# Kernel tuning notes

Measured on AMD Instinct MI355X. Metric: run time of the kernel, lower is better.

## Reference

```python
import jax, jax.numpy as jnp
import numpy as np

BSZ, T, D_IN, P, H, D_OUT = 8, 4096, 512, 256, 256, 512


def setup_inputs() -> dict:
    key = jax.random.key(0)
    ks = jax.random.split(key, 8)
    x_seq = jax.random.normal(ks[0], (BSZ, T, D_IN), dtype=jnp.float32)
    # stable diagonal transition: |a| < 1 so the 4096-step recurrence does not blow up
    a = jax.random.uniform(ks[1], (H,), minval=-0.99, maxval=0.99, dtype=jnp.float32)
    B = jax.random.normal(ks[2], (P, H), dtype=jnp.float32) * 0.05
    C = jax.random.normal(ks[3], (H, P), dtype=jnp.float32) * 0.05
    Wi = jax.random.normal(ks[4], (P, D_IN), dtype=jnp.float32) * 0.05
    bi = jax.random.normal(ks[5], (P,), dtype=jnp.float32) * 0.05
    Wo = jax.random.normal(ks[6], (D_OUT, P), dtype=jnp.float32) * 0.05
    bo = jax.random.normal(ks[7], (D_OUT,), dtype=jnp.float32) * 0.05
    return {"x_seq": x_seq, "a": a, "B": B, "C": C, "Wi": Wi, "bi": bi, "Wo": Wo, "bo": bo}


def reference(x_seq, a, B, C, Wi, bi, Wo, bo):
    # proj_in + relu (eqx.nn.Linear: y = W @ x + b), vmapped over batch and time
    x_proj = jax.nn.relu(jnp.einsum("btd,pd->btp", x_seq, Wi) + bi)  # [Bsz,T,P]
    # precompute driving input u_t = B^T x_t for every step
    u = jnp.einsum("btp,ph->bth", x_proj, B)  # [Bsz,T,H]
    u_t = jnp.swapaxes(u, 0, 1)  # [T,Bsz,H] (scan over time)

    def step(h, u_step):  # h: [Bsz,H]
        h = a * h + u_step
        return h, h

    h0 = jnp.zeros((x_seq.shape[0], a.shape[0]), dtype=x_seq.dtype)
    _, hs = jax.lax.scan(step, h0, u_t)  # hs: [T,Bsz,H]
    # y_t = C^T h_t, then proj_out
    y_seq = jnp.einsum("tbh,hp->btp", hs, C)  # [Bsz,T,P]
    y_out = jnp.einsum("btp,op->bto", y_seq, Wo) + bo  # [Bsz,T,D_out]
    return y_out
```

## Files before the change

### kernel.cpp

```cpp
#include <hip/hip_runtime.h>

#define BSZN 8
#define TT 4096
#define DIN 512
#define PP 256
#define HHH 256
#define DOUT 512
#define LCH 64
#define NCH (TT / LCH)
#define NBLK (BSZN * NCH)
#define XPS 264
#define AST 136

typedef __attribute__((ext_vector_type(8))) short bf16x8;
typedef __attribute__((ext_vector_type(4))) float f32x4;

#define GLOBAL_AS __attribute__((address_space(1)))
#define LDS_AS __attribute__((address_space(3)))

static __device__ __forceinline__ void gld_lds16(const void* g, void* l) {
  __builtin_amdgcn_global_load_lds((const GLOBAL_AS unsigned int*)g,
                                   (LDS_AS unsigned int*)l, 16, 0, 0);
}

static __device__ __forceinline__ unsigned short f2bf(float x) {
  union { float f; unsigned u; } t{x};
  unsigned r = t.u + 0x7fffu + ((t.u >> 16) & 1u);
  return (unsigned short)(r >> 16);
}


__global__ __launch_bounds__(256) void prep_k(
    const float* __restrict__ Wi, const float* __restrict__ Wo,
    const float* __restrict__ Cm, const float* __restrict__ Bm,
    unsigned short* __restrict__ Wi_t, unsigned short* __restrict__ B_t,
    unsigned short* __restrict__ C_t, unsigned short* __restrict__ Wo_t) {
  const int b = blockIdx.x, tid = threadIdx.x;
  if (b < 128) {
    const int idx = b * 1024 + tid * 4;
    const int row = idx >> 9, d = idx & 511;
    const float4 v = *(const float4*)(Wi + idx);
    uint2 w;
    w.x = (unsigned)f2bf(v.x) | ((unsigned)f2bf(v.y) << 16);
    w.y = (unsigned)f2bf(v.z) | ((unsigned)f2bf(v.w) << 16);
    const int tile = d >> 5, kc = (d >> 3) & 3, s = (kc + (row >> 1)) & 3;
    *(uint2*)(Wi_t + tile * 8192 + row * 32 + s * 8 + (d & 7)) = w;
  } else if (b < 192) {
    const int f = (b - 128) * 256 + tid;
    const int p = f >> 6, h = (f & 63) * 4;
    const float4 v = *(const float4*)(Bm + (size_t)p * HHH + h);
    const float vv[4] = {v.x, v.y, v.z, v.w};
    const int tile = p >> 5, kc = (p >> 3) & 3;
#pragma unroll
    for (int j = 0; j < 4; ++j) {
      const int row = h + j, s = (kc + (row >> 1)) & 3;
      B_t[tile * 8192 + row * 32 + s * 8 + (p & 7)] = f2bf(vv[j]);
    }
  } else if (b < 256) {
    const int f = (b - 192) * 256 + tid;
    const int h = f >> 6, p = (f & 63) * 4;
    const float4 v = *(const float4*)(Cm + (size_t)h * PP + p);
    const float vv[4] = {v.x, v.y, v.z, v.w};
    const int tile = h >> 5, kc = (h >> 3) & 3;
#pragma unroll
    for (int j = 0; j < 4; ++j) {
      const int row = p + j, s = (kc + (row >> 1)) & 3;
      C_t[tile * 8192 + row * 32 + s * 8 + (h & 7)] = f2bf(vv[j]);
    }
  } else {
    const int idx = (b - 256) * 1024 + tid * 4;
    const int o = idx >> 8, p = idx & 255;
    const float4 v = *(const float4*)(Wo + idx);
    uint2 w;
    w.x = (unsigned)f2bf(v.x) | ((unsigned)f2bf(v.y) << 16);
    w.y = (unsigned)f2bf(v.z) | ((unsigned)f2bf(v.w) << 16);
    const int tile = p >> 5, kc = (p >> 3) & 3, s = (kc + (o >> 1)) & 3;
    *(uint2*)(Wo_t + tile * 16384 + o * 32 + s * 8 + (p & 7)) = w;
  }
}

__global__ __launch_bounds__(256, 2) void s4_scan(
    const float* __restrict__ x, const float* __restrict__ a,
    const unsigned short* __restrict__ Wi_t, const float* __restrict__ bi,
    const unsigned short* __restrict__ B_t, float* __restrict__ hs0_g,
    float* __restrict__ carry_g) {
  __shared__ alignas(16) char smem[66560];
  char* As = smem;
  unsigned short* xp = (unsigned short*)smem;
  char* TB = smem + 33792;

  const int tid = threadIdx.x, wave = tid >> 6, lane = tid & 63;
  const int l15 = lane & 15, q = lane >> 4;
  const int bc = blockIdx.x;
  const size_t row0 = (size_t)bc * LCH;
  const int wc = wave * 64;

  int wrot[4];
#pragma unroll
  for (int ni = 0; ni < 4; ++ni) {
    const int r = wc + ni * 16 + l15;
    wrot[ni] = r * 64 + (((q + (r >> 1)) & 3) << 4);
  }
  int afb[4];
#pragma unroll
  for (int mi = 0; mi < 4; ++mi) afb[mi] = (mi * 16 + l15) * AST + q * 16;
  int xpb[4];
#pragma unroll
  for (int mi = 0; mi < 4; ++mi) xpb[mi] = (mi * 16 + l15) * XPS + q * 8;

  const int sbase = wave * 4096 + lane * 16;

  f32x4 acc[4][4];
#pragma unroll
  for (int i = 0; i < 4; ++i)
#pragma unroll
    for (int j = 0; j < 4; ++j) acc[i][j] = f32x4{0.f, 0.f, 0.f, 0.f};

  float4 xv[4];
#pragma unroll
  for (int i = 0; i < 4; ++i) {
    const int f = i * 256 + tid;
    xv[i] = *(const float4*)(x + (row0 + (f >> 4)) * DIN + (f & 15) * 4);
  }
  for (int t = 0; t < 8; ++t) {
#pragma unroll
    for (int i = 0; i < 4; ++i) {
      const int f = i * 256 + tid;
      uint2 w;
      w.x = (unsigned)f2bf(xv[i].x) | ((unsigned)f2bf(xv[i].y) << 16);
      w.y = (unsigned)f2bf(xv[i].z) | ((unsigned)f2bf(xv[i].w) << 16);
      *(uint2*)(As + (f >> 4) * AST + (f & 15) * 8) = w;
    }
    {
      const char* gw = (const char*)Wi_t + t * 32768 + sbase;
#pragma unroll
      for (int i = 0; i < 4; ++i) {
        gld_lds16(gw + i * 1024, TB + sbase + i * 1024);
        gld_lds16(gw + 16384 + i * 1024, TB + 16384 + sbase + i * 1024);
      }
    }
    __syncthreads();
    if (t < 7) {
#pragma unroll
      for (int i = 0; i < 4; ++i) {
        const int f = i * 256 + tid;
        xv[i] = *(const float4*)(x + (row0 + (f >> 4)) * DIN + (t + 1) * 64 +
                                 (f & 15) * 4);
      }
    }
    bf16x8 af[4][2], bfv[4][2];
#pragma unroll
    for (int mi = 0; mi < 4; ++mi) {
      af[mi][0] = *(const bf16x8*)(As + afb[mi]);
      af[mi][1] = *(const bf16x8*)(As + afb[mi] + 64);
    }
#pragma unroll
    for (int ni = 0; ni < 4; ++ni) {
      bfv[ni][0] = *(const bf16x8*)(TB + wrot[ni]);
      bfv[ni][1] = *(const bf16x8*)(TB + 16384 + wrot[ni]);
    }
#pragma unroll
    for (int kk = 0; kk < 2; ++kk)
#pragma unroll
      for (int mi = 0; mi < 4; ++mi)
#pragma unroll
        for (int ni = 0; ni < 4; ++ni)
          acc[mi][ni] = __builtin_amdgcn_mfma_f32_16x16x32_bf16(
              af[mi][kk], bfv[ni][kk], acc[mi][ni], 0, 0, 0);
    __syncthreads();
  }

  {
    const char* gw = (const char*)B_t + sbase;
#pragma unroll
    for (int i = 0; i < 4; ++i) {
      gld_lds16(gw + i * 1024, TB + sbase + i * 1024);
      gld_lds16(gw + 16384 + i * 1024, TB + 16384 + sbase + i * 1024);
    }
  }

#pragma unroll
  for (int ni = 0; ni < 4; ++ni) {
    const int col = wc + ni * 16 + l15;
    const float bb = bi[col];
#pragma unroll
    for (int mi = 0; mi < 4; ++mi)
#pragma unroll
      for (int reg = 0; reg < 4; ++reg) {
        const int row = mi * 16 + q * 4 + reg;
        xp[row * XPS + col] = f2bf(fmaxf(acc[mi][ni][reg] + bb, 0.f));
      }
  }

#pragma unroll
  for (int i = 0; i < 4; ++i)
#pragma unroll
    for (int j = 0; j < 4; ++j) acc[i][j] = f32x4{0.f, 0.f, 0.f, 0.f};
  for (int t = 0; t < 4; ++t) {
    if (t > 0) {
      const char* gw = (const char*)B_t + t * 32768 + sbase;
#pragma unroll
      for (int i = 0; i < 4; ++i) {
        gld_lds16(gw + i * 1024, TB + sbase + i * 1024);
        gld_lds16(gw + 16384 + i * 1024, TB + 16384 + sbase + i * 1024);
      }
    }
    __syncthreads();
    bf16x8 af[4][2], bfv[4][2];
#pragma unroll
    for (int mi = 0; mi < 4; ++mi) {
      af[mi][0] = *(const bf16x8*)(xp + xpb[mi] + t * 64);
      af[mi][1] = *(const bf16x8*)(xp + xpb[mi] + t * 64 + 32);
    }
#pragma unroll
    for (int ni = 0; ni < 4; ++ni) {
      bfv[ni][0] = *(const bf16x8*)(TB + wrot[ni]);
      bfv[ni][1] = *(const bf16x8*)(TB + 16384 + wrot[ni]);
    }
#pragma unroll
    for (int kk = 0; kk < 2; ++kk)
#pragma unroll
      for (int mi = 0; mi < 4; ++mi)
#pragma unroll
        for (int ni = 0; ni < 4; ++ni)
          acc[mi][ni] = __builtin_amdgcn_mfma_f32_16x16x32_bf16(
              af[mi][kk], bfv[ni][kk], acc[mi][ni], 0, 0, 0);
    __syncthreads();
  }

  float aC[4], Wz[4];
#pragma unroll
  for (int ni = 0; ni < 4; ++ni) aC[ni] = a[wc + ni * 16 + l15];
#pragma unroll
  for (int ni = 0; ni < 4; ++ni) {
    const float A = aC[ni];
    const float A2 = A * A, A4 = A2 * A2, A8 = A4 * A4, A16 = A8 * A8;
    const float A4q = ((q & 1) ? A4 : 1.f) * ((q & 2) ? A8 : 1.f);
    float W = 0.f;
#pragma unroll
    for (int mi = 0; mi < 4; ++mi) {
      f32x4 v = acc[mi][ni];
      v.y = fmaf(A, v.x, v.y);
      v.z = fmaf(A, v.y, v.z);
      v.w = fmaf(A, v.z, v.w);
      const float E = v.w;
      const float E0 = __shfl(E, l15, 64);
      const float E1 = __shfl(E, l15 + 16, 64);
      const float E2 = __shfl(E, l15 + 32, 64);
      const float E3 = __shfl(E, l15 + 48, 64);
      const float s1 = E0, s2 = fmaf(A4, s1, E1), s3 = fmaf(A4, s2, E2);
      const float s4 = fmaf(A4, s3, E3);
      const float Sq = (q == 0) ? 0.f : (q == 1) ? s1 : (q == 2) ? s2 : s3;
      const float sin_ = fmaf(A4q, W, Sq);
      v.x = fmaf(A, sin_, v.x);
      v.y = fmaf(A2, sin_, v.y);
      v.z = fmaf(A2 * A, sin_, v.z);
      v.w = fmaf(A4, sin_, v.w);
      acc[mi][ni] = v;
      W = fmaf(A16, W, s4);
    }
    Wz[ni] = W;
  }
  if (q == 0) {
#pragma unroll
    for (int ni = 0; ni < 4; ++ni)
      carry_g[(size_t)bc * HHH + wc + ni * 16 + l15] = Wz[ni];
  }
#pragma unroll
  for (int ni = 0; ni < 4; ++ni) {
    const int col = wc + ni * 16 + l15;
#pragma unroll
    for (int mi = 0; mi < 4; ++mi)
#pragma unroll
      for (int reg = 0; reg < 4; ++reg) {
        const int row = mi * 16 + q * 4 + reg;
        hs0_g[(row0 + row) * HHH + col] = acc[mi][ni][reg];
      }
  }
}

__global__ __launch_bounds__(256) void s4_prefix(
    const float* __restrict__ a, const float* __restrict__ carry_g,
    float* __restrict__ P_g) {
  const int b = blockIdx.x, t = threadIdx.x;
  float A = a[t];
#pragma unroll
  for (int j = 0; j < 6; ++j) A *= A;
  const float* cg = carry_g + (size_t)b * NCH * HHH + t;
  float* pg = P_g + (size_t)b * NCH * HHH + t;
  float cv[NCH];
#pragma unroll
  for (int c = 0; c < NCH; ++c) cv[c] = cg[(size_t)c * HHH];
  float P = 0.f;
#pragma unroll
  for (int c = 0; c < NCH; ++c) {
    pg[(size_t)c * HHH] = P;
    P = fmaf(A, P, cv[c]);
  }
}

__global__ __launch_bounds__(256, 2) void s4_out(
    const float* __restrict__ a, const float* __restrict__ hs0_g,
    const float* __restrict__ P_g, const unsigned short* __restrict__ C_t,
    const unsigned short* __restrict__ Wo_t, const float* __restrict__ bo,
    float* __restrict__ out) {
  __shared__ alignas(16) char smem[66560];
  unsigned short* hsL = (unsigned short*)smem;
  char* TB = smem + 33792;

  const int tid = threadIdx.x, wave = tid >> 6, lane = tid & 63;
  const int l15 = lane & 15, q = lane >> 4;
  const int bc = blockIdx.x;
  const size_t row0 = (size_t)bc * LCH;
  const int wc = wave * 64;

  int wrot[4];
#pragma unroll
  for (int ni = 0; ni < 4; ++ni) {
    const int r = wc + ni * 16 + l15;
    wrot[ni] = r * 64 + (((q + (r >> 1)) & 3) << 4);
  }
  int crot[2][4];
#pragma unroll
  for (int g = 0; g < 2; ++g)
#pragma unroll
    for (int ni = 0; ni < 4; ++ni) {
      const int r = wave * 128 + g * 64 + ni * 16 + l15;
      crot[g][ni] = r * 64 + (((q + (r >> 1)) & 3) << 4);
    }
  int xpb[4];
#pragma unroll
  for (int mi = 0; mi < 4; ++mi) xpb[mi] = (mi * 16 + l15) * XPS + q * 8;

  const int sbase = wave * 4096 + lane * 16;

  {
    const char* gw = (const char*)C_t + sbase;
#pragma unroll
    for (int i = 0; i < 4; ++i) {
      gld_lds16(gw + i * 1024, TB + sbase + i * 1024);
      gld_lds16(gw + 16384 + i * 1024, TB + 16384 + sbase + i * 1024);
    }
  }

  f32x4 acc[4][4];
#pragma unroll
  for (int ni = 0; ni < 4; ++ni) {
    const int col = wc + ni * 16 + l15;
#pragma unroll
    for (int mi = 0; mi < 4; ++mi)
#pragma unroll
      for (int reg = 0; reg < 4; ++reg)
        acc[mi][ni][reg] = hs0_g[(row0 + mi * 16 + q * 4 + reg) * HHH + col];
  }
#pragma unroll
  for (int ni = 0; ni < 4; ++ni) {
    const int col = wc + ni * 16 + l15;
    const float A = a[col];
    const float P = P_g[(size_t)bc * HHH + col];
    const float A2 = A * A, A4 = A2 * A2, A8 = A4 * A4, A16 = A8 * A8;
    const float A4q = ((q & 1) ? A4 : 1.f) * ((q & 2) ? A8 : 1.f);
    float fm = A4q * A * P;
#pragma unroll
    for (int mi = 0; mi < 4; ++mi) {
      f32x4 v = acc[mi][ni];
      v.x += fm;
      v.y = fmaf(A, fm, v.y);
      v.z = fmaf(A2, fm, v.z);
      v.w = fmaf(A2 * A, fm, v.w);
      acc[mi][ni] = v;
      fm *= A16;
    }
  }
#pragma unroll
  for (int ni = 0; ni < 4; ++ni) {
    const int col = wc + ni * 16 + l15;
#pragma unroll
    for (int mi = 0; mi < 4; ++mi)
#pragma unroll
      for (int reg = 0; reg < 4; ++reg)
        hsL[(mi * 16 + q * 4 + reg) * XPS + col] = f2bf(acc[mi][ni][reg]);
  }

#pragma unroll
  for (int i = 0; i < 4; ++i)
#pragma unroll
    for (int j = 0; j < 4; ++j) acc[i][j] = f32x4{0.f, 0.f, 0.f, 0.f};
  for (int t = 0; t < 4; ++t) {
    if (t > 0) {
      const char* gw = (const char*)C_t + t * 32768 + sbase;
#pragma unroll
      for (int i = 0; i < 4; ++i) {
        gld_lds16(gw + i * 1024, TB + sbase + i * 1024);
        gld_lds16(gw + 16384 + i * 1024, TB + 16384 + sbase + i * 1024);
      }
    }
    __syncthreads();
    bf16x8 af[4][2], bfv[4][2];
#pragma unroll
    for (int mi = 0; mi < 4; ++mi) {
      af[mi][0] = *(const bf16x8*)(hsL + xpb[mi] + t * 64);
      af[mi][1] = *(const bf16x8*)(hsL + xpb[mi] + t * 64 + 32);
    }
#pragma unroll
    for (int ni = 0; ni < 4; ++ni) {
      bfv[ni][0] = *(const bf16x8*)(TB + wrot[ni]);
      bfv[ni][1] = *(const bf16x8*)(TB + 16384 + wrot[ni]);
    }
#pragma unroll
    for (int kk = 0; kk < 2; ++kk)
#pragma unroll
      for (int mi = 0; mi < 4; ++mi)
#pragma unroll
        for (int ni = 0; ni < 4; ++ni)
          acc[mi][ni] = __builtin_amdgcn_mfma_f32_16x16x32_bf16(
              af[mi][kk], bfv[ni][kk], acc[mi][ni], 0, 0, 0);
    __syncthreads();
  }

  {
    const char* gw = (const char*)Wo_t + wave * 8192 + lane * 16;
#pragma unroll
    for (int i = 0; i < 8; ++i)
      gld_lds16(gw + i * 1024, TB + wave * 8192 + lane * 16 + i * 1024);
  }
#pragma unroll
  for (int ni = 0; ni < 4; ++ni) {
    const int col = wc + ni * 16 + l15;
#pragma unroll
    for (int mi = 0; mi < 4; ++mi)
#pragma unroll
      for (int reg = 0; reg < 4; ++reg)
        hsL[(mi * 16 + q * 4 + reg) * XPS + col] = f2bf(acc[mi][ni][reg]);
  }

  f32x4 oacc[2][4][4];
#pragma unroll
  for (int g = 0; g < 2; ++g)
#pragma unroll
    for (int i = 0; i < 4; ++i)
#pragma unroll
      for (int j = 0; j < 4; ++j) oacc[g][i][j] = f32x4{0.f, 0.f, 0.f, 0.f};
  for (int t = 0; t < 8; ++t) {
    if (t > 0) {
      const char* gw = (const char*)Wo_t + t * 32768 + wave * 8192 + lane * 16;
#pragma unroll
      for (int i = 0; i < 8; ++i)
        gld_lds16(gw + i * 1024, TB + wave * 8192 + lane * 16 + i * 1024);
    }
    __syncthreads();
    bf16x8 af[4], bfv[2][4];
#pragma unroll
    for (int mi = 0; mi < 4; ++mi)
      af[mi] = *(const bf16x8*)(hsL + xpb[mi] + t * 32);
#pragma unroll
    for (int g = 0; g < 2; ++g)
#pragma unroll
      for (int ni = 0; ni < 4; ++ni)
        bfv[g][ni] = *(const bf16x8*)(TB + crot[g][ni]);
#pragma unroll
    for (int g = 0; g < 2; ++g)
#pragma unroll
      for (int mi = 0; mi < 4; ++mi)
#pragma unroll
        for (int ni = 0; ni < 4; ++ni)
          oacc[g][mi][ni] = __builtin_amdgcn_mfma_f32_16x16x32_bf16(
              af[mi], bfv[g][ni], oacc[g][mi][ni], 0, 0, 0);
    __syncthreads();
  }
#pragma unroll
  for (int g = 0; g < 2; ++g)
#pragma unroll
    for (int ni = 0; ni < 4; ++ni) {
      const int ocol = wave * 128 + g * 64 + ni * 16 + l15;
      const float bb = bo[ocol];
#pragma unroll
      for (int mi = 0; mi < 4; ++mi)
#pragma unroll
        for (int reg = 0; reg < 4; ++reg) {
          const int row = mi * 16 + q * 4 + reg;
          out[(row0 + row) * DOUT + ocol] = oacc[g][mi][ni][reg] + bb;
        }
    }
}

extern "C" void kernel_launch(void* const* d_in, const int* in_sizes, int n_in,
                              void* d_out, int out_size, void* d_ws,
                              size_t ws_size, hipStream_t stream) {
  const float* x  = (const float*)d_in[0];
  const float* a  = (const float*)d_in[1];
  const float* Bm = (const float*)d_in[2];
  const float* Cm = (const float*)d_in[3];
  const float* Wi = (const float*)d_in[4];
  const float* bi = (const float*)d_in[5];
  const float* Wo = (const float*)d_in[6];
  const float* bo = (const float*)d_in[7];
  float* out = (float*)d_out;

  char* ws = (char*)d_ws;
  unsigned short* Wi_t = (unsigned short*)ws; ws += (size_t)PP * DIN * 2;
  unsigned short* B_t  = (unsigned short*)ws; ws += (size_t)HHH * PP * 2;
  unsigned short* C_t  = (unsigned short*)ws; ws += (size_t)HHH * PP * 2;
  unsigned short* Wo_t = (unsigned short*)ws; ws += (size_t)DOUT * PP * 2;
  float* carry_g = (float*)ws; ws += (size_t)NBLK * HHH * 4;
  float* P_g     = (float*)ws; ws += (size_t)NBLK * HHH * 4;
  float* hs0_g   = (float*)ws;

  prep_k<<<384, 256, 0, stream>>>(Wi, Wo, Cm, Bm, Wi_t, B_t, C_t, Wo_t);
  s4_scan<<<NBLK, 256, 0, stream>>>(x, a, Wi_t, bi, B_t, hs0_g, carry_g);
  s4_prefix<<<BSZN, 256, 0, stream>>>(a, carry_g, P_g);
  s4_out<<<NBLK, 256, 0, stream>>>(a, hs0_g, P_g, C_t, Wo_t, bo, out);
}
```

Baseline: 172.5 us.

## Read GEMM weight fragments directly from global memory instead of staging through LDS

Removes the global_load_lds staging of the Wi, B, C and Wo tiles into shared memory and has each wave read its bf16 weight fragments straight from global memory (L2/L1 cached), dropping the per-k-step barriers. The whole 64x512 x tile is converted to bf16 up front into LDS, and the second kernel's LDS footprint is halved. The hs0 intermediate is also stored in fragment-native f32x4 order for vectorized writes and reads. This trades LDS traffic and synchronization for more global/cache load latency inside the MFMA loops, with no explicit prefetch to hide it.

```diff
diff --git a/kernel.cpp b/kernel.cpp
--- a/kernel.cpp
+++ b/kernel.cpp
@@ -9,19 +9,11 @@
 #define LCH 64
 #define NCH (TT / LCH)
 #define NBLK (BSZN * NCH)
+#define XTS 520
 #define XPS 264
-#define AST 136
 
 typedef __attribute__((ext_vector_type(8))) short bf16x8;
 typedef __attribute__((ext_vector_type(4))) float f32x4;
-
-#define GLOBAL_AS __attribute__((address_space(1)))
-#define LDS_AS __attribute__((address_space(3)))
-
-static __device__ __forceinline__ void gld_lds16(const void* g, void* l) {
-  __builtin_amdgcn_global_load_lds((const GLOBAL_AS unsigned int*)g,
-                                   (LDS_AS unsigned int*)l, 16, 0, 0);
-}
 
 static __device__ __forceinline__ unsigned short f2bf(float x) {
   union { float f; unsigned u; } t{x};
@@ -85,9 +77,8 @@
     const unsigned short* __restrict__ B_t, float* __restrict__ hs0_g,
     float* __restrict__ carry_g) {
   __shared__ alignas(16) char smem[66560];
-  char* As = smem;
+  unsigned short* xs = (unsigned short*)smem;
   unsigned short* xp = (unsigned short*)smem;
-  char* TB = smem + 33792;
 
   const int tid = threadIdx.x, wave = tid >> 6, lane = tid & 63;
   const int l15 = lane & 15, q = lane >> 4;
@@ -101,83 +92,62 @@
     const int r = wc + ni * 16 + l15;
     wrot[ni] = r * 64 + (((q + (r >> 1)) & 3) << 4);
   }
-  int afb[4];
-#pragma unroll
-  for (int mi = 0; mi < 4; ++mi) afb[mi] = (mi * 16 + l15) * AST + q * 16;
+  int xsb[4];
+#pragma unroll
+  for (int mi = 0; mi < 4; ++mi) xsb[mi] = (mi * 16 + l15) * (XTS * 2) + q * 16;
   int xpb[4];
 #pragma unroll
   for (int mi = 0; mi < 4; ++mi) xpb[mi] = (mi * 16 + l15) * XPS + q * 8;
 
-  const int sbase = wave * 4096 + lane * 16;
-
-  f32x4 acc[4][4];
-#pragma unroll
-  for (int i = 0; i < 4; ++i)
-#pragma unroll
-    for (int j = 0; j < 4; ++j) acc[i][j] = f32x4{0.f, 0.f, 0.f, 0.f};
-
-  float4 xv[4];
-#pragma unroll
-  for (int i = 0; i < 4; ++i) {
-    const int f = i * 256 + tid;
-    xv[i] = *(const float4*)(x + (row0 + (f >> 4)) * DIN + (f & 15) * 4);
-  }
-  for (int t = 0; t < 8; ++t) {
-#pragma unroll
-    for (int i = 0; i < 4; ++i) {
-      const int f = i * 256 + tid;
+#pragma unroll
+  for (int rr = 0; rr < 2; ++rr) {
+    float4 xv[16];
+#pragma unroll
+    for (int i = 0; i < 16; ++i) {
+      const int f = rr * 4096 + i * 256 + tid;
+      xv[i] = *(const float4*)(x + (row0 + (f >> 7)) * DIN + (f & 127) * 4);
+    }
+#pragma unroll
+    for (int i = 0; i < 16; ++i) {
+      const int f = rr * 4096 + i * 256 + tid;
       uint2 w;
       w.x = (unsigned)f2bf(xv[i].x) | ((unsigned)f2bf(xv[i].y) << 16);
       w.y = (unsigned)f2bf(xv[i].z) | ((unsigned)f2bf(xv[i].w) << 16);
-      *(uint2*)(As + (f >> 4) * AST + (f & 15) * 8) = w;
-    }
-    {
-      const char* gw = (const char*)Wi_t + t * 32768 + sbase;
-#pragma unroll
-      for (int i = 0; i < 4; ++i) {
-        gld_lds16(gw + i * 1024, TB + sbase + i * 1024);
-        gld_lds16(gw + 16384 + i * 1024, TB + 16384 + sbase + i * 1024);
-      }
-    }
-    __syncthreads();
-    if (t < 7) {
-#pragma unroll
-      for (int i = 0; i < 4; ++i) {
-        const int f = i * 256 + tid;
-        xv[i] = *(const float4*)(x + (row0 + (f >> 4)) * DIN + (t + 1) * 64 +
-                                 (f & 15) * 4);
-      }
-    }
-    bf16x8 af[4][2], bfv[4][2];
-#pragma unroll
-    for (int mi = 0; mi < 4; ++mi) {
-      af[mi][0] = *(const bf16x8*)(As + afb[mi]);
-      af[mi][1] = *(const bf16x8*)(As + afb[mi] + 64);
-    }
-#pragma unroll
-    for (int ni = 0; ni < 4; ++ni) {
-      bfv[ni][0] = *(const bf16x8*)(TB + wrot[ni]);
-      bfv[ni][1] = *(const bf16x8*)(TB + 16384 + wrot[ni]);
-    }
-#pragma unroll
-    for (int kk = 0; kk < 2; ++kk)
-#pragma unroll
-      for (int mi = 0; mi < 4; ++mi)
-#pragma unroll
-        for (int ni = 0; ni < 4; ++ni)
-          acc[mi][ni] = __builtin_amdgcn_mfma_f32_16x16x32_bf16(
-              af[mi][kk], bfv[ni][kk], acc[mi][ni], 0, 0, 0);
-    __syncthreads();
-  }
-
+      *(uint2*)(xs + (f >> 7) * XTS + (f & 127) * 4) = w;
+    }
+  }
+  __syncthreads();
+
+  f32x4 acc[4][4];
+#pragma unroll
+  for (int i = 0; i < 4; ++i)
+#pragma unroll
+    for (int j = 0; j < 4; ++j) acc[i][j] = f32x4{0.f, 0.f, 0.f, 0.f};
   {
-    const char* gw = (const char*)B_t + sbase;
-#pragma unroll
-    for (int i = 0; i < 4; ++i) {
-      gld_lds16(gw + i * 1024, TB + sbase + i * 1024);
-      gld_lds16(gw + 16384 + i * 1024, TB + 16384 + sbase + i * 1024);
-    }
-  }
+    const char* WiB = (const char*)Wi_t;
+    for (int t = 0; t < 8; ++t) {
+      bf16x8 af[4][2], bfv[4][2];
+#pragma unroll
+      for (int mi = 0; mi < 4; ++mi) {
+        af[mi][0] = *(const bf16x8*)((const char*)xs + xsb[mi] + t * 128);
+        af[mi][1] = *(const bf16x8*)((const char*)xs + xsb[mi] + t * 128 + 64);
+      }
+#pragma unroll
+      for (int ni = 0; ni < 4; ++ni) {
+        bfv[ni][0] = *(const bf16x8*)(WiB + t * 32768 + wrot[ni]);
+        bfv[ni][1] = *(const bf16x8*)(WiB + t * 32768 + 16384 + wrot[ni]);
+      }
+#pragma unroll
+      for (int kk = 0; kk < 2; ++kk)
+#pragma unroll
+        for (int mi = 0; mi < 4; ++mi)
+#pragma unroll
+          for (int ni = 0; ni < 4; ++ni)
+            acc[mi][ni] = __builtin_amdgcn_mfma_f32_16x16x32_bf16(
+                af[mi][kk], bfv[ni][kk], acc[mi][ni], 0, 0, 0);
+    }
+  }
+  __syncthreads();
 
 #pragma unroll
   for (int ni = 0; ni < 4; ++ni) {
@@ -191,41 +161,35 @@
         xp[row * XPS + col] = f2bf(fmaxf(acc[mi][ni][reg] + bb, 0.f));
       }
   }
+  __syncthreads();
 
 #pragma unroll
   for (int i = 0; i < 4; ++i)
 #pragma unroll
     for (int j = 0; j < 4; ++j) acc[i][j] = f32x4{0.f, 0.f, 0.f, 0.f};
-  for (int t = 0; t < 4; ++t) {
-    if (t > 0) {
-      const char* gw = (const char*)B_t + t * 32768 + sbase;
-#pragma unroll
-      for (int i = 0; i < 4; ++i) {
-        gld_lds16(gw + i * 1024, TB + sbase + i * 1024);
-        gld_lds16(gw + 16384 + i * 1024, TB + 16384 + sbase + i * 1024);
-      }
-    }
-    __syncthreads();
-    bf16x8 af[4][2], bfv[4][2];
-#pragma unroll
-    for (int mi = 0; mi < 4; ++mi) {
-      af[mi][0] = *(const bf16x8*)(xp + xpb[mi] + t * 64);
-      af[mi][1] = *(const bf16x8*)(xp + xpb[mi] + t * 64 + 32);
-    }
-#pragma unroll
-    for (int ni = 0; ni < 4; ++ni) {
-      bfv[ni][0] = *(const bf16x8*)(TB + wrot[ni]);
-      bfv[ni][1] = *(const bf16x8*)(TB + 16384 + wrot[ni]);
-    }
-#pragma unroll
-    for (int kk = 0; kk < 2; ++kk)
-#pragma unroll
-      for (int mi = 0; mi < 4; ++mi)
-#pragma unroll
-        for (int ni = 0; ni < 4; ++ni)
-          acc[mi][ni] = __builtin_amdgcn_mfma_f32_16x16x32_bf16(
-              af[mi][kk], bfv[ni][kk], acc[mi][ni], 0, 0, 0);
-    __syncthreads();
+  {
+    const char* BB = (const char*)B_t;
+    for (int t = 0; t < 4; ++t) {
+      bf16x8 af[4][2], bfv[4][2];
+#pragma unroll
+      for (int mi = 0; mi < 4; ++mi) {
+        af[mi][0] = *(const bf16x8*)(xp + xpb[mi] + t * 64);
+        af[mi][1] = *(const bf16x8*)(xp + xpb[mi] + t * 64 + 32);
+      }
+#pragma unroll
+      for (int ni = 0; ni < 4; ++ni) {
+        bfv[ni][0] = *(const bf16x8*)(BB + t * 32768 + wrot[ni]);
+        bfv[ni][1] = *(const bf16x8*)(BB + t * 32768 + 16384 + wrot[ni]);
+      }
+#pragma unroll
+      for (int kk = 0; kk < 2; ++kk)
+#pragma unroll
+        for (int mi = 0; mi < 4; ++mi)
+#pragma unroll
+          for (int ni = 0; ni < 4; ++ni)
+            acc[mi][ni] = __builtin_amdgcn_mfma_f32_16x16x32_bf16(
+                af[mi][kk], bfv[ni][kk], acc[mi][ni], 0, 0, 0);
+    }
   }
 
   float aC[4], Wz[4];
@@ -267,16 +231,13 @@
       carry_g[(size_t)bc * HHH + wc + ni * 16 + l15] = Wz[ni];
   }
 #pragma unroll
-  for (int ni = 0; ni < 4; ++ni) {
-    const int col = wc + ni * 16 + l15;
-#pragma unroll
-    for (int mi = 0; mi < 4; ++mi)
-#pragma unroll
-      for (int reg = 0; reg < 4; ++reg) {
-        const int row = mi * 16 + q * 4 + reg;
-        hs0_g[(row0 + row) * HHH + col] = acc[mi][ni][reg];
-      }
-  }
+  for (int ni = 0; ni < 4; ++ni)
+#pragma unroll
+    for (int mi = 0; mi < 4; ++mi) {
+      const size_t idx =
+          ((((size_t)bc * 4 + wave) * 16 + ni * 4 + mi) * 64 + lane) * 4;
+      *(f32x4*)(hs0_g + idx) = acc[mi][ni];
+    }
 }
 
 __global__ __launch_bounds__(256) void s4_prefix(
@@ -304,9 +265,8 @@
     const float* __restrict__ P_g, const unsigned short* __restrict__ C_t,
     const unsigned short* __restrict__ Wo_t, const float* __restrict__ bo,
     float* __restrict__ out) {
-  __shared__ alignas(16) char smem[66560];
+  __shared__ alignas(16) char smem[33792];
   unsigned short* hsL = (unsigned short*)smem;
-  char* TB = smem + 33792;
 
   const int tid = threadIdx.x, wave = tid >> 6, lane = tid & 63;
   const int l15 = lane & 15, q = lane >> 4;
@@ -332,27 +292,15 @@
 #pragma unroll
   for (int mi = 0; mi < 4; ++mi) xpb[mi] = (mi * 16 + l15) * XPS + q * 8;
 
-  const int sbase = wave * 4096 + lane * 16;
-
-  {
-    const char* gw = (const char*)C_t + sbase;
-#pragma unroll
-    for (int i = 0; i < 4; ++i) {
-      gld_lds16(gw + i * 1024, TB + sbase + i * 1024);
-      gld_lds16(gw + 16384 + i * 1024, TB + 16384 + sbase + i * 1024);
-    }
-  }
-
   f32x4 acc[4][4];
 #pragma unroll
-  for (int ni = 0; ni < 4; ++ni) {
-    const int col = wc + ni * 16 + l15;
-#pragma unroll
-    for (int mi = 0; mi < 4; ++mi)
-#pragma unroll
-      for (int reg = 0; reg < 4; ++reg)
-        acc[mi][ni][reg] = hs0_g[(row0 + mi * 16 + q * 4 + reg) * HHH + col];
-  }
+  for (int ni = 0; ni < 4; ++ni)
+#pragma unroll
+    for (int mi = 0; mi < 4; ++mi) {
+      const size_t idx =
+          ((((size_t)bc * 4 + wave) * 16 + ni * 4 + mi) * 64 + lane) * 4;
+      acc[mi][ni] = *(const f32x4*)(hs0_g + idx);
+    }
 #pragma unroll
   for (int ni = 0; ni < 4; ++ni) {
     const int col = wc + ni * 16 + l15;
@@ -381,49 +329,38 @@
       for (int reg = 0; reg < 4; ++reg)
         hsL[(mi * 16 + q * 4 + reg) * XPS + col] = f2bf(acc[mi][ni][reg]);
   }
+  __syncthreads();
 
 #pragma unroll
   for (int i = 0; i < 4; ++i)
 #pragma unroll
     for (int j = 0; j < 4; ++j) acc[i][j] = f32x4{0.f, 0.f, 0.f, 0.f};
-  for (int t = 0; t < 4; ++t) {
-    if (t > 0) {
-      const char* gw = (const char*)C_t + t * 32768 + sbase;
-#pragma unroll
-      for (int i = 0; i < 4; ++i) {
-        gld_lds16(gw + i * 1024, TB + sbase + i * 1024);
-        gld_lds16(gw + 16384 + i * 1024, TB + 16384 + sbase + i * 1024);
-      }
-    }
-    __syncthreads();
-    bf16x8 af[4][2], bfv[4][2];
-#pragma unroll
-    for (int mi = 0; mi < 4; ++mi) {
-      af[mi][0] = *(const bf16x8*)(hsL + xpb[mi] + t * 64);
-      af[mi][1] = *(const bf16x8*)(hsL + xpb[mi] + t * 64 + 32);
-    }
-#pragma unroll
-    for (int ni = 0; ni < 4; ++ni) {
-      bfv[ni][0] = *(const bf16x8*)(TB + wrot[ni]);
-      bfv[ni][1] = *(const bf16x8*)(TB + 16384 + wrot[ni]);
-    }
-#pragma unroll
-    for (int kk = 0; kk < 2; ++kk)
-#pragma unroll
-      for (int mi = 0; mi < 4; ++mi)
-#pragma unroll
-        for (int ni = 0; ni < 4; ++ni)
-          acc[mi][ni] = __builtin_amdgcn_mfma_f32_16x16x32_bf16(
-              af[mi][kk], bfv[ni][kk], acc[mi][ni], 0, 0, 0);
-    __syncthreads();
-  }
-
   {
-    const char* gw = (const char*)Wo_t + wave * 8192 + lane * 16;
-#pragma unroll
-    for (int i = 0; i < 8; ++i)
-      gld_lds16(gw + i * 1024, TB + wave * 8192 + lane * 16 + i * 1024);
-  }
+    const char* CB = (const char*)C_t;
+    for (int t = 0; t < 4; ++t) {
+      bf16x8 af[4][2], bfv[4][2];
+#pragma unroll
+      for (int mi = 0; mi < 4; ++mi) {
+        af[mi][0] = *(const bf16x8*)(hsL + xpb[mi] + t * 64);
+        af[mi][1] = *(const bf16x8*)(hsL + xpb[mi] + t * 64 + 32);
+      }
+#pragma unroll
+      for (int ni = 0; ni < 4; ++ni) {
+        bfv[ni][0] = *(const bf16x8*)(CB + t * 32768 + wrot[ni]);
+        bfv[ni][1] = *(const bf16x8*)(CB + t * 32768 + 16384 + wrot[ni]);
+      }
+#pragma unroll
+      for (int kk = 0; kk < 2; ++kk)
+#pragma unroll
+        for (int mi = 0; mi < 4; ++mi)
+#pragma unroll
+          for (int ni = 0; ni < 4; ++ni)
+            acc[mi][ni] = __builtin_amdgcn_mfma_f32_16x16x32_bf16(
+                af[mi][kk], bfv[ni][kk], acc[mi][ni], 0, 0, 0);
+    }
+  }
+  __syncthreads();
+
 #pragma unroll
   for (int ni = 0; ni < 4; ++ni) {
     const int col = wc + ni * 16 + l15;
@@ -433,6 +370,7 @@
       for (int reg = 0; reg < 4; ++reg)
         hsL[(mi * 16 + q * 4 + reg) * XPS + col] = f2bf(acc[mi][ni][reg]);
   }
+  __syncthreads();
 
   f32x4 oacc[2][4][4];
 #pragma unroll
@@ -441,32 +379,27 @@
     for (int i = 0; i < 4; ++i)
 #pragma unroll
       for (int j = 0; j < 4; ++j) oacc[g][i][j] = f32x4{0.f, 0.f, 0.f, 0.f};
-  for (int t = 0; t < 8; ++t) {
-    if (t > 0) {
-      const char* gw = (const char*)Wo_t + t * 32768 + wave * 8192 + lane * 16;
-#pragma unroll
-      for (int i = 0; i < 8; ++i)
-        gld_lds16(gw + i * 1024, TB + wave * 8192 + lane * 16 + i * 1024);
-    }
-    __syncthreads();
-    bf16x8 af[4], bfv[2][4];
-#pragma unroll
-    for (int mi = 0; mi < 4; ++mi)
-      af[mi] = *(const bf16x8*)(hsL + xpb[mi] + t * 32);
-#pragma unroll
-    for (int g = 0; g < 2; ++g)
-#pragma unroll
-      for (int ni = 0; ni < 4; ++ni)
-        bfv[g][ni] = *(const bf16x8*)(TB + crot[g][ni]);
-#pragma unroll
-    for (int g = 0; g < 2; ++g)
+  {
+    const char* WoB = (const char*)Wo_t;
+    for (int t = 0; t < 8; ++t) {
+      bf16x8 af[4], bfv[2][4];
 #pragma unroll
       for (int mi = 0; mi < 4; ++mi)
+        af[mi] = *(const bf16x8*)(hsL + xpb[mi] + t * 32);
+#pragma unroll
+      for (int g = 0; g < 2; ++g)
 #pragma unroll
         for (int ni = 0; ni < 4; ++ni)
-          oacc[g][mi][ni] = __builtin_amdgcn_mfma_f32_16x16x32_bf16(
-              af[mi], bfv[g][ni], oacc[g][mi][ni], 0, 0, 0);
-    __syncthreads();
+          bfv[g][ni] = *(const bf16x8*)(WoB + t * 32768 + crot[g][ni]);
+#pragma unroll
+      for (int g = 0; g < 2; ++g)
+#pragma unroll
+        for (int mi = 0; mi < 4; ++mi)
+#pragma unroll
+          for (int ni = 0; ni < 4; ++ni)
+            oacc[g][mi][ni] = __builtin_amdgcn_mfma_f32_16x16x32_bf16(
+                af[mi], bfv[g][ni], oacc[g][mi][ni], 0, 0, 0);
+    }
   }
 #pragma unroll
   for (int g = 0; g < 2; ++g)
```

Result: faster. 161.4 us (-6.5%).
